# Performance work log

Hardware: AMD Instinct MI355X
Metric: run time of the kernel (lower is better)

The kernel has to match this reference:

```python
import jax, jax.numpy as jnp
import numpy as np

N, E, IN, HID, OUT = 100000, 1600000, 128, 128, 64


def setup_inputs() -> dict:
    key = jax.random.key(0)
    ks = jax.random.split(key, 8)
    x = jax.random.normal(ks[0], (N, IN), dtype=jnp.float32)
    edge_index = jax.random.randint(ks[1], (2, E), 0, N, dtype=jnp.int64)
    s = lambda fan_in: 1.0 / np.sqrt(fan_in)
    W1_l = jax.random.normal(ks[2], (IN, HID), dtype=jnp.float32) * s(IN)
    W1_r = jax.random.normal(ks[3], (IN, HID), dtype=jnp.float32) * s(IN)
    b1 = jnp.zeros((HID,), dtype=jnp.float32)
    W2_l = jax.random.normal(ks[4], (HID, OUT), dtype=jnp.float32) * s(HID)
    W2_r = jax.random.normal(ks[5], (HID, OUT), dtype=jnp.float32) * s(HID)
    b2 = jnp.zeros((OUT,), dtype=jnp.float32)
    return {"x": x, "edge_index": edge_index, "W1_l": W1_l, "W1_r": W1_r,
            "b1": b1, "W2_l": W2_l, "W2_r": W2_r, "b2": b2}


def sage_conv(x, src, dst, W_l, W_r, b):
    """PyG SAGEConv (aggr='mean', root_weight=True): lin_l(mean_agg) + lin_r(x)."""
    n = x.shape[0]
    msg = x[src]                                              # [E, d] gather
    agg = jax.ops.segment_sum(msg, dst, num_segments=n)       # [N, d] scatter-add
    deg = jax.ops.segment_sum(jnp.ones_like(dst, dtype=x.dtype), dst,
                              num_segments=n)                 # [N]
    mean = agg / jnp.maximum(deg, 1.0)[:, None]
    return mean @ W_l + x @ W_r + b


def reference(x, edge_index, W1_l, W1_r, b1, W2_l, W2_r, b2):
    src, dst = edge_index[0], edge_index[1]
    h = sage_conv(x, src, dst, W1_l, W1_r, b1)
    h = jax.nn.relu(h)
    # dropout(p=0.5) is identity in eval mode
    out = sage_conv(h, src, dst, W2_l, W2_r, b2)
    return out
```

## Files before the change

### kernel.cpp

```cpp
#include <hip/hip_runtime.h>

#define NN 100000
#define NE 1600000
#define PSHIFT 9
#define PSZ 512
#define NP ((NN + PSZ - 1) / PSZ)
#define BCHUNK 8192
#define NBIN ((NE + BCHUNK - 1) / BCHUNK)
#define SRCMASK 0x1FFFF
#define BUCKET 9216
#define GMTILES ((NN + 63) / 64)
#define GEMM_GB 512

typedef __attribute__((ext_vector_type(8))) short short8;
typedef __attribute__((ext_vector_type(4))) float f32x4;

__device__ __forceinline__ ushort f2bf(float f) {
    uint u = __float_as_uint(f);
    return (ushort)((u + 0x7FFFu + ((u >> 16) & 1u)) >> 16);
}
__device__ __forceinline__ float bflo(uint u) { return __uint_as_float(u << 16); }
__device__ __forceinline__ float bfhi(uint u) { return __uint_as_float(u & 0xffff0000u); }
__device__ __forceinline__ uint packbf(float a, float b) {
    return (uint)f2bf(a) | ((uint)f2bf(b) << 16);
}

__global__ __launch_bounds__(256) void k_prep(const float* __restrict__ W1l,
                                              const float* __restrict__ W1r,
                                              const float* __restrict__ W2l,
                                              const float* __restrict__ W2r,
                                              ushort* __restrict__ WbT1,
                                              ushort* __restrict__ WbT2,
                                              int* __restrict__ gcur)
{
    const int tid = threadIdx.x;
    if (blockIdx.x == 0) {
        if (tid < NP) gcur[tid] = tid * BUCKET;
        return;
    }
    int i = (blockIdx.x - 1) * 256 + tid;
    if (i < 256 * 128) {
        int c = i >> 7, k = i & 127;
        float v = (c < 128) ? W1l[k * 128 + c] : W1r[k * 128 + (c - 128)];
        WbT1[i] = f2bf(v);
    } else if (i < 256 * 128 + 128 * 128) {
        int j = i - 256 * 128;
        int c = j >> 7, k = j & 127;
        float v = (c < 64) ? W2l[k * 64 + c] : W2r[k * 64 + (c - 64)];
        WbT2[j] = f2bf(v);
    }
}

__global__ __launch_bounds__(256) void k_binning(const int* __restrict__ src,
                                                 const int* __restrict__ dst,
                                                 int* __restrict__ gcur,
                                                 uint* __restrict__ packed)
{
    __shared__ int cnt[256];
    __shared__ int base[256];
    const int tid = threadIdx.x;
    const long e0 = (long)blockIdx.x * BCHUNK;
    cnt[tid] = 0;
    __syncthreads();
    for (int i = tid; i < BCHUNK; i += 256) {
        long e = e0 + i;
        if (e < NE) atomicAdd(&cnt[dst[e] >> PSHIFT], 1);
    }
    __syncthreads();
    if (cnt[tid] > 0) base[tid] = atomicAdd(&gcur[tid], cnt[tid]);
    cnt[tid] = 0;
    __syncthreads();
    for (int i = tid; i < BCHUNK; i += 256) {
        long e = e0 + i;
        if (e < NE) {
            int d = dst[e], s = src[e];
            int p = d >> PSHIFT;
            int ofs = atomicAdd(&cnt[p], 1);
            packed[base[p] + ofs] = (uint)s | ((uint)(d & (PSZ - 1)) << 17);
        }
    }
}

__global__ __launch_bounds__(256) void k_pfill(const uint* __restrict__ packed,
                                               const int* __restrict__ gcur,
                                               int* __restrict__ rowptr,
                                               int* __restrict__ rowend,
                                               int* __restrict__ col)
{
    __shared__ int cnt[PSZ];
    __shared__ int cur[PSZ];
    __shared__ int tot[256];
    const int p   = blockIdx.x;
    const int tid = threadIdx.x;
    const int beg = p * BUCKET, end = gcur[p];
    cnt[tid] = 0; cnt[tid + 256] = 0;
    __syncthreads();
    for (int i = beg + tid; i < end; i += 256)
        atomicAdd(&cnt[packed[i] >> 17], 1);
    __syncthreads();
    int v0 = cnt[tid * 2], v1 = cnt[tid * 2 + 1];
    int s  = v0 + v1;
    tot[tid] = s;
    __syncthreads();
    for (int off = 1; off < 256; off <<= 1) {
        int t = (tid >= off) ? tot[tid - off] : 0;
        __syncthreads();
        tot[tid] += t;
        __syncthreads();
    }
    int ex = tot[tid] - s + beg;
    cur[tid * 2]     = ex;
    cur[tid * 2 + 1] = ex + v0;
    int n0 = p * PSZ;
    if (n0 + tid * 2 < NN) {
        rowptr[n0 + tid * 2] = ex;
        rowend[n0 + tid * 2] = ex + v0;
    }
    if (n0 + tid * 2 + 1 < NN) {
        rowptr[n0 + tid * 2 + 1] = ex + v0;
        rowend[n0 + tid * 2 + 1] = ex + v0 + v1;
    }
    __syncthreads();
    for (int i = beg + tid; i < end; i += 256) {
        uint v = packed[i];
        int pos = atomicAdd(&cur[v >> 17], 1);
        col[pos] = (int)(v & SRCMASK);
    }
}

template <bool AF32, int CB, bool YF32>
__global__ __launch_bounds__(512) void k_gemm(const void* __restrict__ Ap,
                                              const ushort* __restrict__ Bt,
                                              const float* __restrict__ bias,
                                              ushort* __restrict__ zb,
                                              void* __restrict__ yout)
{
    constexpr int ZW = CB * 64;
    __shared__ ushort As[2][64 * 128];

    const int tid  = threadIdx.x;
    const int wid  = tid >> 6, lane = tid & 63;
    const int lr   = lane & 15;
    const int lk   = (lane >> 4) << 3;

    short8 bfr[4][CB];
#pragma unroll
    for (int ks = 0; ks < 4; ++ks)
#pragma unroll
        for (int nf = 0; nf < CB; ++nf) {
            int colB = wid * (16 * CB) + nf * 16 + lr;
            bfr[ks][nf] = *reinterpret_cast<const short8*>(
                Bt + (size_t)colB * 128 + ks * 32 + lk);
        }

    const int p0 = tid * 16, p1 = p0 + 8192;
    const int r0 = p0 >> 8, r1 = p1 >> 8;
    const int d0 = p0 ^ ((r0 & 7) << 4);
    const int d1 = p1 ^ ((r1 & 7) << 4);
    const int e0 = (p0 & 255) >> 1;
    const int e1 = (p1 & 255) >> 1;

    const short8 zero8 = {0, 0, 0, 0, 0, 0, 0, 0};
    short8 sA0, sA1;

    auto loadA = [&](int gr, int eo) -> short8 {
        if (gr >= NN) return zero8;
        if (AF32) {
            const float* A = (const float*)Ap;
            float4 f0 = *reinterpret_cast<const float4*>(A + (size_t)gr * 128 + eo);
            float4 f1 = *reinterpret_cast<const float4*>(A + (size_t)gr * 128 + eo + 4);
            short8 v;
            v[0] = (short)f2bf(f0.x); v[1] = (short)f2bf(f0.y);
            v[2] = (short)f2bf(f0.z); v[3] = (short)f2bf(f0.w);
            v[4] = (short)f2bf(f1.x); v[5] = (short)f2bf(f1.y);
            v[6] = (short)f2bf(f1.z); v[7] = (short)f2bf(f1.w);
            return v;
        } else {
            const ushort* A = (const ushort*)Ap;
            return *reinterpret_cast<const short8*>(A + (size_t)gr * 128 + eo);
        }
    };

    int t = blockIdx.x;
    sA0 = loadA(t * 64 + r0, e0);
    sA1 = loadA(t * 64 + r1, e1);

    int cur = 0;
    for (; t < GMTILES; t += GEMM_GB) {
        char* wbase = reinterpret_cast<char*>(As[cur]);
        *reinterpret_cast<short8*>(wbase + d0) = sA0;
        *reinterpret_cast<short8*>(wbase + d1) = sA1;
        __syncthreads();

        int tn = t + GEMM_GB;
        if (tn < GMTILES) {
            sA0 = loadA(tn * 64 + r0, e0);
            sA1 = loadA(tn * 64 + r1, e1);
        }

        f32x4 acc[4][CB];
#pragma unroll
        for (int mi = 0; mi < 4; ++mi)
#pragma unroll
            for (int nf = 0; nf < CB; ++nf) acc[mi][nf] = f32x4{0.f, 0.f, 0.f, 0.f};

        const char* pA = reinterpret_cast<const char*>(As[cur]);
#pragma unroll
        for (int ks = 0; ks < 4; ++ks) {
            int k2 = (ks * 32 + lk) * 2;
            short8 a[4];
#pragma unroll
            for (int mi = 0; mi < 4; ++mi) {
                int r = mi * 16 + lr;
                int byte = (r * 256 + k2) ^ ((r & 7) << 4);
                a[mi] = *reinterpret_cast<const short8*>(pA + byte);
            }
#pragma unroll
            for (int mi = 0; mi < 4; ++mi)
#pragma unroll
                for (int nf = 0; nf < CB; ++nf)
                    acc[mi][nf] = __builtin_amdgcn_mfma_f32_16x16x32_bf16(
                        a[mi], bfr[ks][nf], acc[mi][nf], 0, 0, 0);
        }

#pragma unroll
        for (int mi = 0; mi < 4; ++mi) {
#pragma unroll
            for (int nf = 0; nf < CB; ++nf) {
                int colg = wid * (16 * CB) + nf * 16 + lr;
#pragma unroll
                for (int rr = 0; rr < 4; ++rr) {
                    int rowg = t * 64 + mi * 16 + ((lane >> 4) << 2) + rr;
                    if (rowg < NN) {
                        float v = acc[mi][nf][rr];
                        if (colg < ZW) {
                            zb[(size_t)rowg * ZW + colg] = f2bf(v);
                        } else {
                            int c2 = colg - ZW;
                            if (YF32) ((float*)yout)[(size_t)rowg * ZW + c2]  = v + bias[c2];
                            else      ((ushort*)yout)[(size_t)rowg * ZW + c2] = f2bf(v + bias[c2]);
                        }
                    }
                }
            }
        }
        cur ^= 1;
    }
}

__global__ __launch_bounds__(256) void k_gather1(const ushort* __restrict__ z1b,
                                                 const ushort* __restrict__ y1b,
                                                 const int* __restrict__ rowptr,
                                                 const int* __restrict__ rowend,
                                                 const int* __restrict__ col,
                                                 ushort* __restrict__ hb)
{
    const int w = threadIdx.x >> 6, lane = threadIdx.x & 63;
    const int n = blockIdx.x * 4 + w;
    if (n >= NN) return;
    const int quar = lane >> 4, li = lane & 15;
    const int beg = rowptr[n], end = rowend[n];
    const uint4* zu = (const uint4*)z1b;
    float a0 = 0.f, a1 = 0.f, a2 = 0.f, a3 = 0.f;
    float a4 = 0.f, a5 = 0.f, a6 = 0.f, a7 = 0.f;
    int e = beg;
    for (; e + 15 < end; e += 16) {
        int s0 = col[e      + quar];
        int s1 = col[e + 4  + quar];
        int s2 = col[e + 8  + quar];
        int s3 = col[e + 12 + quar];
        uint4 u0 = zu[(size_t)s0 * 16 + li];
        uint4 u1 = zu[(size_t)s1 * 16 + li];
        uint4 u2 = zu[(size_t)s2 * 16 + li];
        uint4 u3 = zu[(size_t)s3 * 16 + li];
        a0 += bflo(u0.x) + bflo(u1.x) + bflo(u2.x) + bflo(u3.x);
        a1 += bfhi(u0.x) + bfhi(u1.x) + bfhi(u2.x) + bfhi(u3.x);
        a2 += bflo(u0.y) + bflo(u1.y) + bflo(u2.y) + bflo(u3.y);
        a3 += bfhi(u0.y) + bfhi(u1.y) + bfhi(u2.y) + bfhi(u3.y);
        a4 += bflo(u0.z) + bflo(u1.z) + bflo(u2.z) + bflo(u3.z);
        a5 += bfhi(u0.z) + bfhi(u1.z) + bfhi(u2.z) + bfhi(u3.z);
        a6 += bflo(u0.w) + bflo(u1.w) + bflo(u2.w) + bflo(u3.w);
        a7 += bfhi(u0.w) + bfhi(u1.w) + bfhi(u2.w) + bfhi(u3.w);
    }
    for (; e + 3 < end; e += 4) {
        int s0 = col[e + quar];
        uint4 u0 = zu[(size_t)s0 * 16 + li];
        a0 += bflo(u0.x); a1 += bfhi(u0.x);
        a2 += bflo(u0.y); a3 += bfhi(u0.y);
        a4 += bflo(u0.z); a5 += bfhi(u0.z);
        a6 += bflo(u0.w); a7 += bfhi(u0.w);
    }
    int rem = end - e;
    if (quar < rem) {
        int s0 = col[e + quar];
        uint4 u0 = zu[(size_t)s0 * 16 + li];
        a0 += bflo(u0.x); a1 += bfhi(u0.x);
        a2 += bflo(u0.y); a3 += bfhi(u0.y);
        a4 += bflo(u0.z); a5 += bfhi(u0.z);
        a6 += bflo(u0.w); a7 += bfhi(u0.w);
    }
    a0 += __shfl_xor(a0, 16); a1 += __shfl_xor(a1, 16);
    a2 += __shfl_xor(a2, 16); a3 += __shfl_xor(a3, 16);
    a4 += __shfl_xor(a4, 16); a5 += __shfl_xor(a5, 16);
    a6 += __shfl_xor(a6, 16); a7 += __shfl_xor(a7, 16);
    a0 += __shfl_xor(a0, 32); a1 += __shfl_xor(a1, 32);
    a2 += __shfl_xor(a2, 32); a3 += __shfl_xor(a3, 32);
    a4 += __shfl_xor(a4, 32); a5 += __shfl_xor(a5, 32);
    a6 += __shfl_xor(a6, 32); a7 += __shfl_xor(a7, 32);
    if (quar == 0) {
        float inv = 1.0f / (float)max(end - beg, 1);
        uint4 uy = ((const uint4*)y1b)[(size_t)n * 16 + li];
        uint4 o;
        o.x = packbf(fmaxf(a0 * inv + bflo(uy.x), 0.f), fmaxf(a1 * inv + bfhi(uy.x), 0.f));
        o.y = packbf(fmaxf(a2 * inv + bflo(uy.y), 0.f), fmaxf(a3 * inv + bfhi(uy.y), 0.f));
        o.z = packbf(fmaxf(a4 * inv + bflo(uy.z), 0.f), fmaxf(a5 * inv + bfhi(uy.z), 0.f));
        o.w = packbf(fmaxf(a6 * inv + bflo(uy.w), 0.f), fmaxf(a7 * inv + bfhi(uy.w), 0.f));
        ((uint4*)hb)[(size_t)n * 16 + li] = o;
    }
}

__global__ __launch_bounds__(256) void k_gather2(const ushort* __restrict__ z2b,
                                                 const ushort* __restrict__ y2b,
                                                 const int* __restrict__ rowptr,
                                                 const int* __restrict__ rowend,
                                                 const int* __restrict__ col,
                                                 float* __restrict__ out)
{
    const int w = threadIdx.x >> 6, lane = threadIdx.x & 63;
    const int n = blockIdx.x * 4 + w;
    if (n >= NN) return;
    const int quar = lane >> 4, li = lane & 15;
    const int beg = rowptr[n], end = rowend[n];
    const uint2* zu = (const uint2*)z2b;
    float a0 = 0.f, a1 = 0.f, a2 = 0.f, a3 = 0.f;
    int e = beg;
    for (; e + 15 < end; e += 16) {
        int s0 = col[e      + quar];
        int s1 = col[e + 4  + quar];
        int s2 = col[e + 8  + quar];
        int s3 = col[e + 12 + quar];
        uint2 u0 = zu[(size_t)s0 * 16 + li];
        uint2 u1 = zu[(size_t)s1 * 16 + li];
        uint2 u2 = zu[(size_t)s2 * 16 + li];
        uint2 u3 = zu[(size_t)s3 * 16 + li];
        a0 += bflo(u0.x) + bflo(u1.x) + bflo(u2.x) + bflo(u3.x);
        a1 += bfhi(u0.x) + bfhi(u1.x) + bfhi(u2.x) + bfhi(u3.x);
        a2 += bflo(u0.y) + bflo(u1.y) + bflo(u2.y) + bflo(u3.y);
        a3 += bfhi(u0.y) + bfhi(u1.y) + bfhi(u2.y) + bfhi(u3.y);
    }
    for (; e + 3 < end; e += 4) {
        int s0 = col[e + quar];
        uint2 u0 = zu[(size_t)s0 * 16 + li];
        a0 += bflo(u0.x); a1 += bfhi(u0.x);
        a2 += bflo(u0.y); a3 += bfhi(u0.y);
    }
    int rem = end - e;
    if (quar < rem) {
        int s0 = col[e + quar];
        uint2 u0 = zu[(size_t)s0 * 16 + li];
        a0 += bflo(u0.x); a1 += bfhi(u0.x);
        a2 += bflo(u0.y); a3 += bfhi(u0.y);
    }
    a0 += __shfl_xor(a0, 16); a1 += __shfl_xor(a1, 16);
    a2 += __shfl_xor(a2, 16); a3 += __shfl_xor(a3, 16);
    a0 += __shfl_xor(a0, 32); a1 += __shfl_xor(a1, 32);
    a2 += __shfl_xor(a2, 32); a3 += __shfl_xor(a3, 32);
    if (quar == 0) {
        float inv = 1.0f / (float)max(end - beg, 1);
        uint2 uy = ((const uint2*)y2b)[(size_t)n * 16 + li];
        float4 o;
        o.x = a0 * inv + bflo(uy.x);
        o.y = a1 * inv + bfhi(uy.x);
        o.z = a2 * inv + bflo(uy.y);
        o.w = a3 * inv + bfhi(uy.y);
        ((float4*)out)[(size_t)n * 16 + li] = o;
    }
}

extern "C" void kernel_launch(void* const* d_in, const int* in_sizes, int n_in,
                              void* d_out, int out_size, void* d_ws, size_t ws_size,
                              hipStream_t stream)
{
    const float* x   = (const float*)d_in[0];
    const int*   ei  = (const int*)d_in[1];
    const float* W1l = (const float*)d_in[2];
    const float* W1r = (const float*)d_in[3];
    const float* b1  = (const float*)d_in[4];
    const float* W2l = (const float*)d_in[5];
    const float* W2r = (const float*)d_in[6];
    const float* b2  = (const float*)d_in[7];
    float* out = (float*)d_out;

    const int* src = ei;
    const int* dst = ei + NE;

    int*  rowptr = (int*)d_ws;
    int*  rowend = rowptr + NN;
    int*  gcur   = rowend + NN;
    uint* packed = (uint*)(gcur + 256);
    int*  colA   = (int*)(packed + (size_t)NP * BUCKET);
    uintptr_t p = (uintptr_t)(colA + (size_t)NP * BUCKET);
    p = (p + 255) & ~(uintptr_t)255;
    ushort* WbT1 = (ushort*)p;  p += (size_t)256 * 128 * 2;
    ushort* WbT2 = (ushort*)p;  p += (size_t)128 * 128 * 2;
    p = (p + 255) & ~(uintptr_t)255;
    ushort* z1b = (ushort*)p;   p += (size_t)NN * 128 * 2;
    ushort* y1b = (ushort*)p;   p += (size_t)NN * 128 * 2;
    ushort* hb  = (ushort*)p;   p += (size_t)NN * 128 * 2;
    ushort* z2b = z1b;
    ushort* y2b = y1b;

    k_prep<<<1 + (256 * 128 + 128 * 128 + 255) / 256, 256, 0, stream>>>(
        W1l, W1r, W2l, W2r, WbT1, WbT2, gcur);

    k_binning<<<NBIN, 256, 0, stream>>>(src, dst, gcur, packed);
    k_pfill<<<NP, 256, 0, stream>>>(packed, gcur, rowptr, rowend, colA);

    k_gemm<true, 2, false><<<GEMM_GB, 512, 0, stream>>>(x, WbT1, b1, z1b, y1b);
    k_gather1<<<(NN + 3) / 4, 256, 0, stream>>>(z1b, y1b, rowptr, rowend, colA, hb);

    k_gemm<false, 1, false><<<GEMM_GB, 512, 0, stream>>>(hb, WbT2, b2, z2b, y2b);
    k_gather2<<<(NN + 3) / 4, 256, 0, stream>>>(z2b, y2b, rowptr, rowend, colA, out);
}
```

Measured before the change: 237.2 us.

## Prefetch neighbor indices and use packed f32x2 accumulation in gather kernels

Both gather kernels now load the next batch of column indices before accumulating the current batch, overlapping the index load with the feature gathers. Accumulation moves to two-wide float vectors so the compiler can use packed FP32 adds, and the high half of each bf16 pair is added without masking. The root-term load is hoisted to the kernel start. The edge binning chunk size is also halved. This adds register pressure, and unmasked high halves bring small rounding differences.

```diff
diff --git a/kernel.cpp b/kernel.cpp
--- a/kernel.cpp
+++ b/kernel.cpp
@@ -5,7 +5,7 @@
 #define PSHIFT 9
 #define PSZ 512
 #define NP ((NN + PSZ - 1) / PSZ)
-#define BCHUNK 8192
+#define BCHUNK 4096
 #define NBIN ((NE + BCHUNK - 1) / BCHUNK)
 #define SRCMASK 0x1FFFF
 #define BUCKET 9216
@@ -14,6 +14,7 @@
 
 typedef __attribute__((ext_vector_type(8))) short short8;
 typedef __attribute__((ext_vector_type(4))) float f32x4;
+typedef __attribute__((ext_vector_type(2))) float f32x2;
 
 __device__ __forceinline__ ushort f2bf(float f) {
     uint u = __float_as_uint(f);
@@ -23,6 +24,18 @@
 __device__ __forceinline__ float bfhi(uint u) { return __uint_as_float(u & 0xffff0000u); }
 __device__ __forceinline__ uint packbf(float a, float b) {
     return (uint)f2bf(a) | ((uint)f2bf(b) << 16);
+}
+__device__ __forceinline__ void acc2(f32x2& A, uint u) {
+    f32x2 v;
+    v.x = __uint_as_float(u << 16);
+    v.y = __uint_as_float(u);
+    A += v;
+}
+__device__ __forceinline__ void acc2x(f32x2& A, uint u) {
+    f32x2 v;
+    v.x = bflo(u);
+    v.y = bfhi(u);
+    A += v;
 }
 
 __global__ __launch_bounds__(256) void k_prep(const float* __restrict__ W1l,
@@ -261,60 +274,56 @@
     const int quar = lane >> 4, li = lane & 15;
     const int beg = rowptr[n], end = rowend[n];
     const uint4* zu = (const uint4*)z1b;
-    float a0 = 0.f, a1 = 0.f, a2 = 0.f, a3 = 0.f;
-    float a4 = 0.f, a5 = 0.f, a6 = 0.f, a7 = 0.f;
+    uint4 uy = ((const uint4*)y1b)[(size_t)n * 16 + li];
+
+    f32x2 A0 = {0.f, 0.f}, A1 = {0.f, 0.f}, A2 = {0.f, 0.f}, A3 = {0.f, 0.f};
     int e = beg;
-    for (; e + 15 < end; e += 16) {
-        int s0 = col[e      + quar];
-        int s1 = col[e + 4  + quar];
-        int s2 = col[e + 8  + quar];
-        int s3 = col[e + 12 + quar];
-        uint4 u0 = zu[(size_t)s0 * 16 + li];
-        uint4 u1 = zu[(size_t)s1 * 16 + li];
-        uint4 u2 = zu[(size_t)s2 * 16 + li];
-        uint4 u3 = zu[(size_t)s3 * 16 + li];
-        a0 += bflo(u0.x) + bflo(u1.x) + bflo(u2.x) + bflo(u3.x);
-        a1 += bfhi(u0.x) + bfhi(u1.x) + bfhi(u2.x) + bfhi(u3.x);
-        a2 += bflo(u0.y) + bflo(u1.y) + bflo(u2.y) + bflo(u3.y);
-        a3 += bfhi(u0.y) + bfhi(u1.y) + bfhi(u2.y) + bfhi(u3.y);
-        a4 += bflo(u0.z) + bflo(u1.z) + bflo(u2.z) + bflo(u3.z);
-        a5 += bfhi(u0.z) + bfhi(u1.z) + bfhi(u2.z) + bfhi(u3.z);
-        a6 += bflo(u0.w) + bflo(u1.w) + bflo(u2.w) + bflo(u3.w);
-        a7 += bfhi(u0.w) + bfhi(u1.w) + bfhi(u2.w) + bfhi(u3.w);
+    int c0 = 0, c1 = 0, c2 = 0, c3 = 0;
+    bool have = (e + 15 < end);
+    if (have) {
+        c0 = col[e + quar];      c1 = col[e + 4 + quar];
+        c2 = col[e + 8 + quar];  c3 = col[e + 12 + quar];
+    }
+    while (have) {
+        uint4 u0 = zu[(size_t)c0 * 16 + li];
+        uint4 u1 = zu[(size_t)c1 * 16 + li];
+        uint4 u2 = zu[(size_t)c2 * 16 + li];
+        uint4 u3 = zu[(size_t)c3 * 16 + li];
+        e += 16;
+        have = (e + 15 < end);
+        if (have) {
+            c0 = col[e + quar];      c1 = col[e + 4 + quar];
+            c2 = col[e + 8 + quar];  c3 = col[e + 12 + quar];
+        }
+        acc2(A0, u0.x); acc2(A1, u0.y); acc2(A2, u0.z); acc2(A3, u0.w);
+        acc2(A0, u1.x); acc2(A1, u1.y); acc2(A2, u1.z); acc2(A3, u1.w);
+        acc2(A0, u2.x); acc2(A1, u2.y); acc2(A2, u2.z); acc2(A3, u2.w);
+        acc2(A0, u3.x); acc2(A1, u3.y); acc2(A2, u3.z); acc2(A3, u3.w);
     }
     for (; e + 3 < end; e += 4) {
-        int s0 = col[e + quar];
-        uint4 u0 = zu[(size_t)s0 * 16 + li];
-        a0 += bflo(u0.x); a1 += bfhi(u0.x);
-        a2 += bflo(u0.y); a3 += bfhi(u0.y);
-        a4 += bflo(u0.z); a5 += bfhi(u0.z);
-        a6 += bflo(u0.w); a7 += bfhi(u0.w);
+        uint4 u0 = zu[(size_t)col[e + quar] * 16 + li];
+        acc2x(A0, u0.x); acc2x(A1, u0.y); acc2x(A2, u0.z); acc2x(A3, u0.w);
     }
     int rem = end - e;
     if (quar < rem) {
-        int s0 = col[e + quar];
-        uint4 u0 = zu[(size_t)s0 * 16 + li];
-        a0 += bflo(u0.x); a1 += bfhi(u0.x);
-        a2 += bflo(u0.y); a3 += bfhi(u0.y);
-        a4 += bflo(u0.z); a5 += bfhi(u0.z);
-        a6 += bflo(u0.w); a7 += bfhi(u0.w);
-    }
-    a0 += __shfl_xor(a0, 16); a1 += __shfl_xor(a1, 16);
-    a2 += __shfl_xor(a2, 16); a3 += __shfl_xor(a3, 16);
-    a4 += __shfl_xor(a4, 16); a5 += __shfl_xor(a5, 16);
-    a6 += __shfl_xor(a6, 16); a7 += __shfl_xor(a7, 16);
-    a0 += __shfl_xor(a0, 32); a1 += __shfl_xor(a1, 32);
-    a2 += __shfl_xor(a2, 32); a3 += __shfl_xor(a3, 32);
-    a4 += __shfl_xor(a4, 32); a5 += __shfl_xor(a5, 32);
-    a6 += __shfl_xor(a6, 32); a7 += __shfl_xor(a7, 32);
+        uint4 u0 = zu[(size_t)col[e + quar] * 16 + li];
+        acc2x(A0, u0.x); acc2x(A1, u0.y); acc2x(A2, u0.z); acc2x(A3, u0.w);
+    }
+    A0.x += __shfl_xor(A0.x, 16); A0.y += __shfl_xor(A0.y, 16);
+    A1.x += __shfl_xor(A1.x, 16); A1.y += __shfl_xor(A1.y, 16);
+    A2.x += __shfl_xor(A2.x, 16); A2.y += __shfl_xor(A2.y, 16);
+    A3.x += __shfl_xor(A3.x, 16); A3.y += __shfl_xor(A3.y, 16);
+    A0.x += __shfl_xor(A0.x, 32); A0.y += __shfl_xor(A0.y, 32);
+    A1.x += __shfl_xor(A1.x, 32); A1.y += __shfl_xor(A1.y, 32);
+    A2.x += __shfl_xor(A2.x, 32); A2.y += __shfl_xor(A2.y, 32);
+    A3.x += __shfl_xor(A3.x, 32); A3.y += __shfl_xor(A3.y, 32);
     if (quar == 0) {
         float inv = 1.0f / (float)max(end - beg, 1);
-        uint4 uy = ((const uint4*)y1b)[(size_t)n * 16 + li];
         uint4 o;
-        o.x = packbf(fmaxf(a0 * inv + bflo(uy.x), 0.f), fmaxf(a1 * inv + bfhi(uy.x), 0.f));
-        o.y = packbf(fmaxf(a2 * inv + bflo(uy.y), 0.f), fmaxf(a3 * inv + bfhi(uy.y), 0.f));
-        o.z = packbf(fmaxf(a4 * inv + bflo(uy.z), 0.f), fmaxf(a5 * inv + bfhi(uy.z), 0.f));
-        o.w = packbf(fmaxf(a6 * inv + bflo(uy.w), 0.f), fmaxf(a7 * inv + bfhi(uy.w), 0.f));
+        o.x = packbf(fmaxf(A0.x * inv + bflo(uy.x), 0.f), fmaxf(A0.y * inv + bfhi(uy.x), 0.f));
+        o.y = packbf(fmaxf(A1.x * inv + bflo(uy.y), 0.f), fmaxf(A1.y * inv + bfhi(uy.y), 0.f));
+        o.z = packbf(fmaxf(A2.x * inv + bflo(uy.z), 0.f), fmaxf(A2.y * inv + bfhi(uy.z), 0.f));
+        o.w = packbf(fmaxf(A3.x * inv + bflo(uy.w), 0.f), fmaxf(A3.y * inv + bfhi(uy.w), 0.f));
         ((uint4*)hb)[(size_t)n * 16 + li] = o;
     }
 }
@@ -332,47 +341,52 @@
     const int quar = lane >> 4, li = lane & 15;
     const int beg = rowptr[n], end = rowend[n];
     const uint2* zu = (const uint2*)z2b;
-    float a0 = 0.f, a1 = 0.f, a2 = 0.f, a3 = 0.f;
+    uint2 uy = ((const uint2*)y2b)[(size_t)n * 16 + li];
+
+    f32x2 A0 = {0.f, 0.f}, A1 = {0.f, 0.f};
     int e = beg;
-    for (; e + 15 < end; e += 16) {
-        int s0 = col[e      + quar];
-        int s1 = col[e + 4  + quar];
-        int s2 = col[e + 8  + quar];
-        int s3 = col[e + 12 + quar];
-        uint2 u0 = zu[(size_t)s0 * 16 + li];
-        uint2 u1 = zu[(size_t)s1 * 16 + li];
-        uint2 u2 = zu[(size_t)s2 * 16 + li];
-        uint2 u3 = zu[(size_t)s3 * 16 + li];
-        a0 += bflo(u0.x) + bflo(u1.x) + bflo(u2.x) + bflo(u3.x);
-        a1 += bfhi(u0.x) + bfhi(u1.x) + bfhi(u2.x) + bfhi(u3.x);
-        a2 += bflo(u0.y) + bflo(u1.y) + bflo(u2.y) + bflo(u3.y);
-        a3 += bfhi(u0.y) + bfhi(u1.y) + bfhi(u2.y) + bfhi(u3.y);
+    int c0 = 0, c1 = 0, c2 = 0, c3 = 0;
+    bool have = (e + 15 < end);
+    if (have) {
+        c0 = col[e + quar];      c1 = col[e + 4 + quar];
+        c2 = col[e + 8 + quar];  c3 = col[e + 12 + quar];
+    }
+    while (have) {
+        uint2 u0 = zu[(size_t)c0 * 16 + li];
+        uint2 u1 = zu[(size_t)c1 * 16 + li];
+        uint2 u2 = zu[(size_t)c2 * 16 + li];
+        uint2 u3 = zu[(size_t)c3 * 16 + li];
+        e += 16;
+        have = (e + 15 < end);
+        if (have) {
+            c0 = col[e + quar];      c1 = col[e + 4 + quar];
+            c2 = col[e + 8 + quar];  c3 = col[e + 12 + quar];
+        }
+        acc2(A0, u0.x); acc2(A1, u0.y);
+        acc2(A0, u1.x); acc2(A1, u1.y);
+        acc2(A0, u2.x); acc2(A1, u2.y);
+        acc2(A0, u3.x); acc2(A1, u3.y);
     }
     for (; e + 3 < end; e += 4) {
-        int s0 = col[e + quar];
-        uint2 u0 = zu[(size_t)s0 * 16 + li];
-        a0 += bflo(u0.x); a1 += bfhi(u0.x);
-        a2 += bflo(u0.y); a3 += bfhi(u0.y);
+        uint2 u0 = zu[(size_t)col[e + quar] * 16 + li];
+        acc2x(A0, u0.x); acc2x(A1, u0.y);
     }
     int rem = end - e;
     if (quar < rem) {
-        int s0 = col[e + quar];
-        uint2 u0 = zu[(size_t)s0 * 16 + li];
-        a0 += bflo(u0.x); a1 += bfhi(u0.x);
-        a2 += bflo(u0.y); a3 += bfhi(u0.y);
-    }
-    a0 += __shfl_xor(a0, 16); a1 += __shfl_xor(a1, 16);
-    a2 += __shfl_xor(a2, 16); a3 += __shfl_xor(a3, 16);
-    a0 += __shfl_xor(a0, 32); a1 += __shfl_xor(a1, 32);
-    a2 += __shfl_xor(a2, 32); a3 += __shfl_xor(a3, 32);
+        uint2 u0 = zu[(size_t)col[e + quar] * 16 + li];
+        acc2x(A0, u0.x); acc2x(A1, u0.y);
+    }
+    A0.x += __shfl_xor(A0.x, 16); A0.y += __shfl_xor(A0.y, 16);
+    A1.x += __shfl_xor(A1.x, 16); A1.y += __shfl_xor(A1.y, 16);
+    A0.x += __shfl_xor(A0.x, 32); A0.y += __shfl_xor(A0.y, 32);
+    A1.x += __shfl_xor(A1.x, 32); A1.y += __shfl_xor(A1.y, 32);
     if (quar == 0) {
         float inv = 1.0f / (float)max(end - beg, 1);
-        uint2 uy = ((const uint2*)y2b)[(size_t)n * 16 + li];
         float4 o;
-        o.x = a0 * inv + bflo(uy.x);
-        o.y = a1 * inv + bfhi(uy.x);
-        o.z = a2 * inv + bflo(uy.y);
-        o.w = a3 * inv + bfhi(uy.y);
+        o.x = A0.x * inv + bflo(uy.x);
+        o.y = A0.y * inv + bfhi(uy.x);
+        o.z = A1.x * inv + bflo(uy.y);
+        o.w = A1.y * inv + bfhi(uy.y);
         ((float4*)out)[(size_t)n * 16 + li] = o;
     }
 }
```

Measured after the change: 228.8 us. -3.5%, faster.
